# Kernel optimization log

Measured on AMD Instinct MI355X. Metric: run time of the kernel, lower is better.

Reference implementation:

```python
import jax, jax.numpy as jnp
import numpy as np

B, T, E, H = 4, 1024, 768, 12
HD = E // H                      # 64
R = 2                            # lora rank
LORA_SCALE = 1.0 / R             # loralib default lora_alpha=1 -> alpha/r
NUM_BUCKETS, MAX_DIST = 320, 800


def _rel_bucket(rel):
    nb = NUM_BUCKETS // 2                      # 160
    buckets = (rel > 0).astype(jnp.int32) * nb
    rel = jnp.abs(rel)
    max_exact = nb // 2                        # 80
    is_small = rel < max_exact
    log_ratio = jnp.log(jnp.maximum(rel, 1).astype(jnp.float32) / max_exact)
    large = max_exact + (log_ratio / np.log(MAX_DIST / max_exact) * (nb - max_exact)).astype(jnp.int32)
    large = jnp.minimum(large, nb - 1)
    return buckets + jnp.where(is_small, rel, large)


def setup_inputs() -> dict:
    key = jax.random.key(0)
    ks = jax.random.split(key, 22)
    s = 0.02
    w = lambda k, shape: jax.random.normal(k, shape, jnp.float32) * s
    return {
        "hidden_states": jax.random.normal(ks[0], (B, T, E), jnp.float32),
        "Wq": w(ks[1], (E, E)), "bq": w(ks[2], (E,)),
        "Wk": w(ks[3], (E, E)), "bk": w(ks[4], (E,)),
        "Wv": w(ks[5], (E, E)), "bv": w(ks[6], (E,)),
        "Aq": w(ks[7], (R, E)), "Bq": w(ks[8], (E, R)),
        "Ak": w(ks[9], (R, E)), "Bk": w(ks[10], (E, R)),
        "Av": w(ks[11], (R, E)), "Bv": w(ks[12], (E, R)),
        "Wo": w(ks[13], (E, E)), "bo": w(ks[14], (E,)),
        "Wg": w(ks[15], (8, HD)), "bg": w(ks[16], (8,)),
        "gru_const": jnp.ones((1, H, 1, 1), jnp.float32),
        "rel_embed": w(ks[17], (NUM_BUCKETS, H)),
    }


def reference(hidden_states, Wq, bq, Wk, bk, Wv, bv,
              Aq, Bq, Ak, Bk, Av, Bv, Wo, bo, Wg, bg, gru_const, rel_embed):
    Bsz, Tq, _ = hidden_states.shape
    # --- relative position bias [H, T, T] ---
    pos = jnp.arange(Tq)
    bucket = _rel_bucket(pos[None, :] - pos[:, None])
    pos_bias = rel_embed[bucket].transpose(2, 0, 1)
    # --- dynamic gate from hidden states, per head/position ---
    g = hidden_states.reshape(Bsz, Tq, H, HD).transpose(0, 2, 1, 3)      # [B,H,T,hd]
    gp = jnp.einsum('bhtd,ed->bhte', g, Wg) + bg                          # [B,H,T,8]
    gp = gp.reshape(Bsz, H, Tq, 2, 4).sum(-1)                             # [B,H,T,2]
    gates = jax.nn.sigmoid(gp)
    gate_a, gate_b = gates[..., :1], gates[..., 1:]
    gate = gate_a * (gate_b * gru_const - 1.0) + 2.0                      # [B,H,T,1]
    gated_bias = gate * pos_bias[None]                                    # [B,H,T,T]
    # --- projections: original double-applies q/k/v_proj (proj+LoRA, then
    #     again inside F.multi_head_attention_forward via separate proj weights) ---
    lin = lambda x, W, b: jnp.einsum('bte,oe->bto', x, W) + b
    lora = lambda x, A, Bm: jnp.einsum('bte,re,or->bto', x, A, Bm) * LORA_SCALE
    x = hidden_states
    q1 = lin(x, Wq, bq) + lora(x, Aq, Bq)
    k1 = lin(x, Wk, bk) + lora(x, Ak, Bk)
    v1 = lin(x, Wv, bv) + lora(x, Av, Bv)
    q = lin(q1, Wq, bq) * (HD ** -0.5)
    k = lin(k1, Wk, bk)
    v = lin(v1, Wv, bv)
    qh = q.reshape(Bsz, Tq, H, HD).transpose(0, 2, 1, 3)
    kh = k.reshape(Bsz, Tq, H, HD).transpose(0, 2, 1, 3)
    vh = v.reshape(Bsz, Tq, H, HD).transpose(0, 2, 1, 3)
    scores = jnp.einsum('bhqd,bhkd->bhqk', qh, kh) + gated_bias
    attn = jax.nn.softmax(scores, axis=-1)
    ctx = jnp.einsum('bhqk,bhkd->bhqd', attn, vh)
    out = ctx.transpose(0, 2, 1, 3).reshape(Bsz, Tq, E)
    return jnp.einsum('bte,oe->bto', out, Wo) + bo
```

## Files before the change

### kernel.cpp

```cpp
#include <hip/hip_runtime.h>
#include <math.h>

#define TT 1024
#define EE 768
#define HH 12

typedef __attribute__((ext_vector_type(8))) __bf16 bf16x8;
typedef __attribute__((ext_vector_type(4))) float f32x4;

__device__ __forceinline__ unsigned short f2b(float f) {
    unsigned int u = __float_as_uint(f);
    unsigned int r = (u + 0x7fffu + ((u >> 16) & 1u)) >> 16;
    return (unsigned short)r;
}

#define GLD16(gsrc, ldst) \
    __builtin_amdgcn_global_load_lds( \
        (const __attribute__((address_space(1))) unsigned int*)(gsrc), \
        (__attribute__((address_space(3))) unsigned int*)(ldst), 16, 0, 0)

__global__ __launch_bounds__(256)
void prep_k(const float* __restrict__ hs, const float* __restrict__ Wq,
            const float* __restrict__ Wk, const float* __restrict__ Wv,
            const float* __restrict__ Wo, unsigned short* __restrict__ out) {
    size_t i = 4 * (size_t)(blockIdx.x * 256 + threadIdx.x);
    if (i >= 5505024) return;
    const float* src;
    if (i < 3145728)      src = hs + i;
    else if (i < 3735552) src = Wq + (i - 3145728);
    else if (i < 4325376) src = Wk + (i - 3735552);
    else if (i < 4915200) src = Wv + (i - 4325376);
    else                  src = Wo + (i - 4915200);
    float4 f = *(const float4*)src;
    unsigned int lo = (unsigned int)f2b(f.x) | ((unsigned int)f2b(f.y) << 16);
    unsigned int hi = (unsigned int)f2b(f.z) | ((unsigned int)f2b(f.w) << 16);
    uint2 p; p.x = lo; p.y = hi;
    *(uint2*)&out[i] = p;
}

__global__ void biastab_k(const float* __restrict__ rel_embed,
                          float* __restrict__ biasTab) {
    int idx = blockIdx.x * 256 + threadIdx.x;
    if (idx >= 2047 * 12) return;
    int h = idx % 12;
    int rr = idx / 12;
    int rel = rr - 1023;
    int base = rel > 0 ? 160 : 0;
    int ar = rel < 0 ? -rel : rel;
    int bkt;
    if (ar < 80) {
        bkt = base + ar;
    } else {
        double lr = log((double)ar / 80.0);
        int large = 80 + (int)(lr / log(10.0) * 80.0);
        if (large > 159) large = 159;
        bkt = base + large;
    }
    biasTab[h * 2048 + rr] = rel_embed[bkt * 12 + h];
}

__global__ __launch_bounds__(256)
void gates_k(const float* __restrict__ hs, const float* __restrict__ Wg,
             const float* __restrict__ bg, const float* __restrict__ gru,
             float* __restrict__ gate) {
    __shared__ float WgS[8][64];
    __shared__ float bgS[8];
    __shared__ float gcS[12];
    const int tid = threadIdx.x;
    for (int i = tid; i < 512; i += 256) WgS[i >> 6][i & 63] = Wg[i];
    if (tid < 8)  bgS[tid] = bg[tid];
    if (tid < 12) gcS[tid] = gru[tid];
    __syncthreads();
    int idx = blockIdx.x * 256 + tid;
    int t = idx & 1023;
    int h = (idx >> 10) % 12;
    int b = idx / (12 * 1024);
    const float* gp = hs + ((size_t)(b * TT + t)) * EE + h * 64;
    float acc[8];
    #pragma unroll
    for (int e = 0; e < 8; ++e) acc[e] = 0.f;
    #pragma unroll
    for (int d4 = 0; d4 < 64; d4 += 4) {
        float4 u = *(const float4*)(gp + d4);
        float gv[4] = {u.x, u.y, u.z, u.w};
        #pragma unroll
        for (int j = 0; j < 4; ++j) {
            #pragma unroll
            for (int e = 0; e < 8; ++e) acc[e] += gv[j] * WgS[e][d4 + j];
        }
    }
    float s0 = acc[0] + acc[1] + acc[2] + acc[3] + bgS[0] + bgS[1] + bgS[2] + bgS[3];
    float s1 = acc[4] + acc[5] + acc[6] + acc[7] + bgS[4] + bgS[5] + bgS[6] + bgS[7];
    float ga = 1.f / (1.f + __expf(-s0));
    float gb = 1.f / (1.f + __expf(-s1));
    gate[idx] = ga * (gb * gcS[h] - 1.0f) + 2.0f;
}

__global__ __launch_bounds__(64)
void lora_down_k(const float* __restrict__ x,
                 const float* __restrict__ Aq, const float* __restrict__ Ak,
                 const float* __restrict__ Av, float* __restrict__ xA) {
    const int m = blockIdx.x;
    const int lane = threadIdx.x;
    const float* xp = x + (size_t)m * EE;
    float s[6] = {0.f, 0.f, 0.f, 0.f, 0.f, 0.f};
    for (int c = lane * 4; c < EE; c += 256) {
        float4 u = *(const float4*)(xp + c);
        float xv[4] = {u.x, u.y, u.z, u.w};
        #pragma unroll
        for (int j = 0; j < 4; ++j) {
            int e = c + j;
            s[0] += xv[j] * Aq[e];       s[1] += xv[j] * Aq[EE + e];
            s[2] += xv[j] * Ak[e];       s[3] += xv[j] * Ak[EE + e];
            s[4] += xv[j] * Av[e];       s[5] += xv[j] * Av[EE + e];
        }
    }
    #pragma unroll
    for (int off = 32; off > 0; off >>= 1) {
        #pragma unroll
        for (int i = 0; i < 6; ++i) s[i] += __shfl_down(s[i], off, 64);
    }
    if (lane == 0) {
        const int M2 = 4096 * 2;
        xA[m * 2 + 0] = s[0];            xA[m * 2 + 1] = s[1];
        xA[M2 + m * 2 + 0] = s[2];       xA[M2 + m * 2 + 1] = s[3];
        xA[2 * M2 + m * 2 + 0] = s[4];   xA[2 * M2 + m * 2 + 1] = s[5];
    }
}

template<int MODE>
__global__ __launch_bounds__(256, 2)
void gemm_k(const unsigned short* __restrict__ Aall,
            const unsigned short* __restrict__ W0b, const unsigned short* __restrict__ W1b,
            const unsigned short* __restrict__ W2b,
            const float* __restrict__ b0, const float* __restrict__ b1, const float* __restrict__ b2,
            const float* __restrict__ xA,
            const float* __restrict__ Bm0, const float* __restrict__ Bm1, const float* __restrict__ Bm2,
            void* __restrict__ out) {
    __shared__ unsigned short At[128 * 32];
    __shared__ unsigned short Bt[128 * 32];
    const int tid = threadIdx.x;
    const int bx = blockIdx.x, by = blockIdx.y;

    int sel, row0, col0;
    if (MODE == 0)      { sel = bx / 6;  col0 = (bx % 6) * 128; row0 = by * 128; }
    else if (MODE == 1) { sel = by / 32; col0 = bx * 128;       row0 = by * 128; }
    else                { sel = 0;       col0 = bx * 128;       row0 = by * 128; }
    const unsigned short* Wb = sel == 0 ? W0b : (sel == 1 ? W1b : W2b);
    const float* bias = sel == 0 ? b0 : (sel == 1 ? b1 : b2);
    float scale = (MODE == 1 && sel == 0) ? 0.125f : 1.0f;

    const int lane = tid & 63, wv = tid >> 6;
    const int wm = (wv & 1) * 64, wn = (wv >> 1) * 64;
    const int l15 = lane & 15, g8 = (lane >> 4) * 8;
    const int lr = lane >> 2, lc = (lane & 3) * 8;

    f32x4 zero4 = {0.f, 0.f, 0.f, 0.f};
    f32x4 acc[4][4];
    #pragma unroll
    for (int i = 0; i < 4; ++i)
        #pragma unroll
        for (int j = 0; j < 4; ++j) acc[i][j] = zero4;

    const int c0 = wv * 2, c1 = wv * 2 + 1;
    const unsigned short* Abase0 = Aall + (size_t)(row0 + c0 * 16 + lr) * EE + lc;
    const unsigned short* Abase1 = Aall + (size_t)(row0 + c1 * 16 + lr) * EE + lc;
    const unsigned short* Bbase0 = Wb + (size_t)(col0 + c0 * 16 + lr) * EE + lc;
    const unsigned short* Bbase1 = Wb + (size_t)(col0 + c1 * 16 + lr) * EE + lc;

    for (int kt = 0; kt < 768; kt += 32) {
        GLD16(Abase0 + kt, &At[c0 * 512]);
        GLD16(Abase1 + kt, &At[c1 * 512]);
        GLD16(Bbase0 + kt, &Bt[c0 * 512]);
        GLD16(Bbase1 + kt, &Bt[c1 * 512]);
        __syncthreads();
        bf16x8 af[4], bf[4];
        #pragma unroll
        for (int mt = 0; mt < 4; ++mt) af[mt] = *(const bf16x8*)&At[(wm + mt * 16 + l15) * 32 + g8];
        #pragma unroll
        for (int nt = 0; nt < 4; ++nt) bf[nt] = *(const bf16x8*)&Bt[(wn + nt * 16 + l15) * 32 + g8];
        #pragma unroll
        for (int mt = 0; mt < 4; ++mt)
            #pragma unroll
            for (int nt = 0; nt < 4; ++nt)
                acc[mt][nt] = __builtin_amdgcn_mfma_f32_16x16x32_bf16(af[mt], bf[nt], acc[mt][nt], 0, 0, 0);
        __syncthreads();
    }

    const float* Lbase = (MODE == 0) ? (xA + sel * 8192) : nullptr;
    const float* BmSel = (MODE == 0) ? (sel == 0 ? Bm0 : (sel == 1 ? Bm1 : Bm2)) : nullptr;
    const int g4 = (lane >> 4) * 4;
    #pragma unroll
    for (int mt = 0; mt < 4; ++mt) {
        #pragma unroll
        for (int r = 0; r < 4; ++r) {
            size_t grow = (size_t)row0 + wm + mt * 16 + g4 + r;
            float l0 = 0.f, l1 = 0.f;
            if (MODE == 0) { l0 = Lbase[grow * 2]; l1 = Lbase[grow * 2 + 1]; }
            #pragma unroll
            for (int nt = 0; nt < 4; ++nt) {
                int ncol = col0 + wn + nt * 16 + l15;
                float c = (acc[mt][nt][r] + bias[ncol]) * scale;
                if (MODE == 0) c += 0.5f * (l0 * BmSel[ncol * 2] + l1 * BmSel[ncol * 2 + 1]);
                if (MODE == 0) {
                    ((unsigned short*)out)[(size_t)sel * 4096 * EE + grow * EE + ncol] = f2b(c);
                } else if (MODE == 1) {
                    ((unsigned short*)out)[grow * EE + ncol] = f2b(c);
                } else {
                    ((float*)out)[grow * EE + ncol] = c;
                }
            }
        }
    }
}

__global__ __launch_bounds__(256)
void vT_k(const unsigned short* __restrict__ vb, unsigned short* __restrict__ Vtg) {
    __shared__ unsigned short Vs[64 * 72];
    const int tid = threadIdx.x;
    const int tt = blockIdx.x, h = blockIdx.y, b = blockIdx.z;
    const int r = tid >> 3, cc = (tid & 7) * 8;
    #pragma unroll
    for (int i = 0; i < 2; ++i) {
        int row = i * 32 + r;
        const unsigned short* vp = vb + (size_t)(b * TT + tt * 64 + row) * EE + h * 64 + cc;
        *(uint4*)&Vs[row * 72 + cc] = *(const uint4*)vp;
    }
    __syncthreads();
    #pragma unroll
    for (int i = 0; i < 2; ++i) {
        int d = i * 32 + r;
        unsigned short tmp[8] __attribute__((aligned(16)));
        #pragma unroll
        for (int j = 0; j < 8; ++j) tmp[j] = Vs[(cc + j) * 72 + d];
        *(uint4*)&Vtg[((size_t)(b * HH + h) * 64 + d) * TT + tt * 64 + cc] = *(const uint4*)tmp;
    }
}

__global__ __launch_bounds__(256, 3)
void attn_k(const unsigned short* __restrict__ qb, const unsigned short* __restrict__ kb,
            const unsigned short* __restrict__ Vtg, const float* __restrict__ gate,
            const float* __restrict__ biasTab, unsigned short* __restrict__ ctx) {
    __shared__ unsigned short Qs[64 * 72];
    __shared__ unsigned short Ks[64 * 72];
    __shared__ unsigned short Vt[64 * 72];
    __shared__ unsigned short Ps[64 * 72];
    __shared__ float btabS[2048];
    const int tid = threadIdx.x;
    const int qt = blockIdx.x, h = blockIdx.y, b = blockIdx.z;

    for (int i = tid; i < 2047; i += 256) btabS[i] = biasTab[h * 2048 + i];

    const int srow = tid >> 2, scol = (tid & 3) * 16;
    {
        const unsigned short* qp = qb + ((size_t)(b * TT + qt * 64 + srow)) * EE + h * 64 + scol;
        *(uint4*)&Qs[srow * 72 + scol]     = *(const uint4*)qp;
        *(uint4*)&Qs[srow * 72 + scol + 8] = *(const uint4*)(qp + 8);
    }
    const int lane = tid & 63, wv = tid >> 6;
    const int m0 = wv * 16;
    const int l15 = lane & 15, g = lane >> 4;

    float li[4];
    f32x4 zero4 = {0.f, 0.f, 0.f, 0.f};
    f32x4 oa[4];
    #pragma unroll
    for (int r = 0; r < 4; ++r) li[r] = 0.f;
    #pragma unroll
    for (int nt = 0; nt < 4; ++nt) oa[nt] = zero4;
    float gv[4];
    #pragma unroll
    for (int r = 0; r < 4; ++r)
        gv[r] = gate[((size_t)(b * HH + h)) * TT + qt * 64 + m0 + 4 * g + r];
    const unsigned short* vrow = Vtg + ((size_t)(b * HH + h) * 64 + srow) * TT;
    __syncthreads();

    for (int kt = 0; kt < 16; ++kt) {
        {
            const unsigned short* kp = kb + ((size_t)(b * TT + kt * 64 + srow)) * EE + h * 64 + scol;
            *(uint4*)&Ks[srow * 72 + scol]     = *(const uint4*)kp;
            *(uint4*)&Ks[srow * 72 + scol + 8] = *(const uint4*)(kp + 8);
            const unsigned short* vp = vrow + kt * 64 + scol;
            *(uint4*)&Vt[srow * 72 + scol]     = *(const uint4*)vp;
            *(uint4*)&Vt[srow * 72 + scol + 8] = *(const uint4*)(vp + 8);
        }
        __syncthreads();
        f32x4 sa[4];
        #pragma unroll
        for (int nt = 0; nt < 4; ++nt) sa[nt] = zero4;
        bf16x8 aq0 = *(const bf16x8*)&Qs[(m0 + l15) * 72 + g * 8];
        bf16x8 aq1 = *(const bf16x8*)&Qs[(m0 + l15) * 72 + 32 + g * 8];
        #pragma unroll
        for (int nt = 0; nt < 4; ++nt) {
            bf16x8 bk0 = *(const bf16x8*)&Ks[(nt * 16 + l15) * 72 + g * 8];
            bf16x8 bk1 = *(const bf16x8*)&Ks[(nt * 16 + l15) * 72 + 32 + g * 8];
            sa[nt] = __builtin_amdgcn_mfma_f32_16x16x32_bf16(aq0, bk0, sa[nt], 0, 0, 0);
            sa[nt] = __builtin_amdgcn_mfma_f32_16x16x32_bf16(aq1, bk1, sa[nt], 0, 0, 0);
        }
        #pragma unroll
        for (int nt = 0; nt < 4; ++nt) {
            int ibase = kt * 64 + nt * 16 + l15 + 1023 - qt * 64 - m0 - 4 * g;
            #pragma unroll
            for (int r = 0; r < 4; ++r) {
                float e = __expf(sa[nt][r] + gv[r] * btabS[ibase - r]);
                li[r] += e;
                Ps[(m0 + 4 * g + r) * 72 + nt * 16 + l15] = f2b(e);
            }
        }
        bf16x8 ap0 = *(const bf16x8*)&Ps[(m0 + l15) * 72 + g * 8];
        bf16x8 ap1 = *(const bf16x8*)&Ps[(m0 + l15) * 72 + 32 + g * 8];
        #pragma unroll
        for (int nt = 0; nt < 4; ++nt) {
            bf16x8 bv0 = *(const bf16x8*)&Vt[(nt * 16 + l15) * 72 + g * 8];
            bf16x8 bv1 = *(const bf16x8*)&Vt[(nt * 16 + l15) * 72 + 32 + g * 8];
            oa[nt] = __builtin_amdgcn_mfma_f32_16x16x32_bf16(ap0, bv0, oa[nt], 0, 0, 0);
            oa[nt] = __builtin_amdgcn_mfma_f32_16x16x32_bf16(ap1, bv1, oa[nt], 0, 0, 0);
        }
        __syncthreads();
    }
    #pragma unroll
    for (int r = 0; r < 4; ++r) {
        #pragma unroll
        for (int msk = 1; msk < 16; msk <<= 1)
            li[r] += __shfl_xor(li[r], msk, 16);
    }
    #pragma unroll
    for (int nt = 0; nt < 4; ++nt)
        #pragma unroll
        for (int r = 0; r < 4; ++r)
            Ks[(m0 + 4 * g + r) * 72 + nt * 16 + l15] = f2b(oa[nt][r] / li[r]);
    __syncthreads();
    {
        unsigned short* cp = ctx + ((size_t)(b * TT + qt * 64 + srow)) * EE + h * 64 + scol;
        *(uint4*)cp       = *(const uint4*)&Ks[srow * 72 + scol];
        *(uint4*)(cp + 8) = *(const uint4*)&Ks[srow * 72 + scol + 8];
    }
}

extern "C" void kernel_launch(void* const* d_in, const int* in_sizes, int n_in,
                              void* d_out, int out_size, void* d_ws, size_t ws_size,
                              hipStream_t stream) {
    const float* hs  = (const float*)d_in[0];
    const float* Wq  = (const float*)d_in[1];
    const float* bq  = (const float*)d_in[2];
    const float* Wk  = (const float*)d_in[3];
    const float* bk  = (const float*)d_in[4];
    const float* Wv  = (const float*)d_in[5];
    const float* bv  = (const float*)d_in[6];
    const float* Aq  = (const float*)d_in[7];
    const float* Bq  = (const float*)d_in[8];
    const float* Ak  = (const float*)d_in[9];
    const float* Bk  = (const float*)d_in[10];
    const float* Av  = (const float*)d_in[11];
    const float* Bv  = (const float*)d_in[12];
    const float* Wo  = (const float*)d_in[13];
    const float* bo  = (const float*)d_in[14];
    const float* Wg  = (const float*)d_in[15];
    const float* bg  = (const float*)d_in[16];
    const float* gru = (const float*)d_in[17];
    const float* rel = (const float*)d_in[18];

    float* ws = (float*)d_ws;
    float* gate    = ws;
    float* biasTab = gate + 49152;
    float* xA      = biasTab + 24576;
    unsigned short* hsb   = (unsigned short*)(xA + 24576);
    unsigned short* Wqb   = hsb + 3145728;
    unsigned short* Wkb   = Wqb + 589824;
    unsigned short* Wvb   = Wkb + 589824;
    unsigned short* Wob   = Wvb + 589824;
    unsigned short* qkv1b = Wob + 589824;
    unsigned short* qkvb  = qkv1b + 3 * 3145728;
    unsigned short* ctxb  = qkv1b;
    unsigned short* Vtg   = qkv1b + 3145728;

    prep_k<<<5376, 256, 0, stream>>>(hs, Wq, Wk, Wv, Wo, hsb);
    biastab_k<<<96, 256, 0, stream>>>(rel, biasTab);
    gates_k<<<192, 256, 0, stream>>>(hs, Wg, bg, gru, gate);
    lora_down_k<<<4096, 64, 0, stream>>>(hs, Aq, Ak, Av, xA);

    gemm_k<0><<<dim3(18, 32), 256, 0, stream>>>(hsb, Wqb, Wkb, Wvb, bq, bk, bv,
                                                xA, Bq, Bk, Bv, qkv1b);
    gemm_k<1><<<dim3(6, 96), 256, 0, stream>>>(qkv1b, Wqb, Wkb, Wvb, bq, bk, bv,
                                               nullptr, nullptr, nullptr, nullptr, qkvb);

    vT_k<<<dim3(16, 12, 4), 256, 0, stream>>>(qkvb + 2 * 3145728, Vtg);

    attn_k<<<dim3(16, 12, 4), 256, 0, stream>>>(qkvb, qkvb + 3145728, Vtg,
                                                gate, biasTab, ctxb);

    gemm_k<2><<<dim3(6, 32), 256, 0, stream>>>(ctxb, Wob, Wob, Wob, bo, bo, bo,
                                               nullptr, nullptr, nullptr, nullptr, d_out);
}
```

Measured before the change: 241.4 us.

## Fold double projection into precomputed W·W weights and fuse setup kernels

The two chained q/k/v projections are folded algebraically: W2 = W·W is computed by a small weight GEMM, together with a combined bias W·b+b and LoRA factor W·B, so only one large activation GEMM is needed. The four prep kernels (bf16 convert, bias table, gates, LoRA down) are merged into one multi-role setup kernel. The V transpose is fused into the projection epilogue through strided stores. This removes a full 4096x2304x768 GEMM and several launches, at the cost of a weight-side GEMM per call and extra bf16 rounding of the product weights.

```diff
diff --git a/kernel.cpp b/kernel.cpp
--- a/kernel.cpp
+++ b/kernel.cpp
@@ -20,154 +20,264 @@
         (__attribute__((address_space(3))) unsigned int*)(ldst), 16, 0, 0)
 
 __global__ __launch_bounds__(256)
-void prep_k(const float* __restrict__ hs, const float* __restrict__ Wq,
-            const float* __restrict__ Wk, const float* __restrict__ Wv,
-            const float* __restrict__ Wo, unsigned short* __restrict__ out) {
-    size_t i = 4 * (size_t)(blockIdx.x * 256 + threadIdx.x);
-    if (i >= 5505024) return;
-    const float* src;
-    if (i < 3145728)      src = hs + i;
-    else if (i < 3735552) src = Wq + (i - 3145728);
-    else if (i < 4325376) src = Wk + (i - 3735552);
-    else if (i < 4915200) src = Wv + (i - 4325376);
-    else                  src = Wo + (i - 4915200);
-    float4 f = *(const float4*)src;
-    unsigned int lo = (unsigned int)f2b(f.x) | ((unsigned int)f2b(f.y) << 16);
-    unsigned int hi = (unsigned int)f2b(f.z) | ((unsigned int)f2b(f.w) << 16);
-    uint2 p; p.x = lo; p.y = hi;
-    *(uint2*)&out[i] = p;
-}
-
-__global__ void biastab_k(const float* __restrict__ rel_embed,
-                          float* __restrict__ biasTab) {
-    int idx = blockIdx.x * 256 + threadIdx.x;
-    if (idx >= 2047 * 12) return;
-    int h = idx % 12;
-    int rr = idx / 12;
-    int rel = rr - 1023;
-    int base = rel > 0 ? 160 : 0;
-    int ar = rel < 0 ? -rel : rel;
-    int bkt;
-    if (ar < 80) {
-        bkt = base + ar;
+void setup_k(const float* __restrict__ hs,
+             const float* __restrict__ Wq, const float* __restrict__ Wk,
+             const float* __restrict__ Wv, const float* __restrict__ Wo,
+             const float* __restrict__ bq, const float* __restrict__ bk,
+             const float* __restrict__ bv,
+             const float* __restrict__ Aq, const float* __restrict__ Ak,
+             const float* __restrict__ Av,
+             const float* __restrict__ Bq, const float* __restrict__ Bk,
+             const float* __restrict__ Bv,
+             const float* __restrict__ Wg, const float* __restrict__ bg,
+             const float* __restrict__ gru, const float* __restrict__ rel,
+             unsigned short* __restrict__ hsb, unsigned short* __restrict__ Wall_b,
+             unsigned short* __restrict__ WT_all,
+             float* __restrict__ xA, float* __restrict__ gate,
+             float* __restrict__ biasTab, float* __restrict__ bias2,
+             float* __restrict__ B2) {
+    __shared__ __align__(16) char smem[34816];
+    const int bid = blockIdx.x, tid = threadIdx.x;
+
+    if (bid < 4096) {
+        float* rowF = (float*)smem;
+        float* WgS  = rowF + 768;
+        float* bgS  = WgS + 512;
+        float* gpS  = bgS + 8;
+        float* redS = gpS + 96;
+        const int m = bid;
+        const float* xrow = hs + (size_t)m * EE;
+        if (tid < 192) {
+            float4 f = ((const float4*)xrow)[tid];
+            rowF[tid * 4 + 0] = f.x; rowF[tid * 4 + 1] = f.y;
+            rowF[tid * 4 + 2] = f.z; rowF[tid * 4 + 3] = f.w;
+            unsigned int lo = (unsigned int)f2b(f.x) | ((unsigned int)f2b(f.y) << 16);
+            unsigned int hi = (unsigned int)f2b(f.z) | ((unsigned int)f2b(f.w) << 16);
+            uint2 p; p.x = lo; p.y = hi;
+            *(uint2*)&hsb[(size_t)m * EE + tid * 4] = p;
+        }
+        for (int i = tid; i < 512; i += 256) WgS[i] = Wg[i];
+        if (tid < 8) bgS[tid] = bg[tid];
+        __syncthreads();
+        float s[6] = {0.f, 0.f, 0.f, 0.f, 0.f, 0.f};
+        #pragma unroll
+        for (int j = 0; j < 3; ++j) {
+            int e = tid * 3 + j;
+            float xv = rowF[e];
+            s[0] += xv * Aq[e]; s[1] += xv * Aq[EE + e];
+            s[2] += xv * Ak[e]; s[3] += xv * Ak[EE + e];
+            s[4] += xv * Av[e]; s[5] += xv * Av[EE + e];
+        }
+        #pragma unroll
+        for (int off = 32; off > 0; off >>= 1)
+            #pragma unroll
+            for (int i = 0; i < 6; ++i) s[i] += __shfl_down(s[i], off, 64);
+        if ((tid & 63) == 0)
+            #pragma unroll
+            for (int i = 0; i < 6; ++i) redS[(tid >> 6) * 6 + i] = s[i];
+        if (tid < 96) {
+            int h = tid >> 3, e = tid & 7;
+            float acc = 0.f;
+            #pragma unroll 16
+            for (int d = 0; d < 64; ++d) acc += rowF[h * 64 + d] * WgS[e * 64 + d];
+            gpS[h * 8 + e] = acc + bgS[e];
+        }
+        __syncthreads();
+        if (tid < 6) {
+            float v = redS[tid] + redS[6 + tid] + redS[12 + tid] + redS[18 + tid];
+            int sel = tid >> 1, r = tid & 1;
+            xA[sel * 8192 + m * 2 + r] = v;
+        }
+        if (tid < 12) {
+            int h = tid;
+            float s0 = gpS[h * 8 + 0] + gpS[h * 8 + 1] + gpS[h * 8 + 2] + gpS[h * 8 + 3];
+            float s1 = gpS[h * 8 + 4] + gpS[h * 8 + 5] + gpS[h * 8 + 6] + gpS[h * 8 + 7];
+            float ga = 1.f / (1.f + __expf(-s0));
+            float gb = 1.f / (1.f + __expf(-s1));
+            int b = m >> 10, tp = m & 1023;
+            gate[((size_t)b * HH + h) * TT + tp] = ga * (gb * gru[h] - 1.0f) + 2.0f;
+        }
+    } else if (bid < 5248) {
+        size_t base = (size_t)(bid - 4096) * 2048 + tid * 8;
+        int mat = (int)(base / 589824);
+        size_t local = base % 589824;
+        const float* S = mat == 0 ? Wq : (mat == 1 ? Wk : (mat == 2 ? Wv : Wo));
+        float4 a = *(const float4*)&S[local];
+        float4 c = *(const float4*)&S[local + 4];
+        unsigned short hb[8] __attribute__((aligned(16)));
+        hb[0] = f2b(a.x); hb[1] = f2b(a.y); hb[2] = f2b(a.z); hb[3] = f2b(a.w);
+        hb[4] = f2b(c.x); hb[5] = f2b(c.y); hb[6] = f2b(c.z); hb[7] = f2b(c.w);
+        *(uint4*)&Wall_b[base] = *(const uint4*)hb;
+    } else if (bid < 5356) {
+        unsigned short* Ts = (unsigned short*)smem;
+        int v = bid - 5248;
+        int mat = v / 36, tile = v % 36;
+        int tr = tile / 6, tc = tile % 6;
+        const float* S = mat == 0 ? Wq : (mat == 1 ? Wk : Wv);
+        #pragma unroll
+        for (int i = 0; i < 16; ++i) {
+            int idx = i * 256 + tid;
+            int row = idx >> 5, col4 = (idx & 31) * 4;
+            float4 f = *(const float4*)&S[(size_t)(tr * 128 + row) * EE + tc * 128 + col4];
+            Ts[(col4 + 0) * 136 + row] = f2b(f.x);
+            Ts[(col4 + 1) * 136 + row] = f2b(f.y);
+            Ts[(col4 + 2) * 136 + row] = f2b(f.z);
+            Ts[(col4 + 3) * 136 + row] = f2b(f.w);
+        }
+        __syncthreads();
+        unsigned short* dst = WT_all + (size_t)mat * 589824;
+        #pragma unroll
+        for (int i = 0; i < 8; ++i) {
+            int idx = i * 256 + tid;
+            int rr = idx >> 4, cg = (idx & 15) * 8;
+            *(uint4*)&dst[(size_t)(tc * 128 + rr) * EE + tr * 128 + cg] =
+                *(const uint4*)&Ts[rr * 136 + cg];
+        }
+    } else if (bid < 5452) {
+        int idx = (bid - 5356) * 256 + tid;
+        if (idx < 2047 * 12) {
+            int h = idx % 12;
+            int rr = idx / 12;
+            int relv = rr - 1023;
+            int base = relv > 0 ? 160 : 0;
+            int ar = relv < 0 ? -relv : relv;
+            int bkt;
+            if (ar < 80) bkt = base + ar;
+            else {
+                double lr = log((double)ar / 80.0);
+                int large = 80 + (int)(lr / log(10.0) * 80.0);
+                if (large > 159) large = 159;
+                bkt = base + large;
+            }
+            biasTab[h * 2048 + rr] = rel[bkt * 12 + h];
+        }
     } else {
-        double lr = log((double)ar / 80.0);
-        int large = 80 + (int)(lr / log(10.0) * 80.0);
-        if (large > 159) large = 159;
-        bkt = base + large;
-    }
-    biasTab[h * 2048 + rr] = rel_embed[bkt * 12 + h];
-}
-
-__global__ __launch_bounds__(256)
-void gates_k(const float* __restrict__ hs, const float* __restrict__ Wg,
-             const float* __restrict__ bg, const float* __restrict__ gru,
-             float* __restrict__ gate) {
-    __shared__ float WgS[8][64];
-    __shared__ float bgS[8];
-    __shared__ float gcS[12];
+        float* bvS = (float*)smem;
+        float* BmS = bvS + 768;
+        int v = bid - 5452;
+        int sel = v / 4, nb = (v % 4) * 192;
+        const float* W = sel == 0 ? Wq : (sel == 1 ? Wk : Wv);
+        const float* bvec = sel == 0 ? bq : (sel == 1 ? bk : bv);
+        const float* Bm = sel == 0 ? Bq : (sel == 1 ? Bk : Bv);
+        for (int i = tid; i < 768; i += 256) bvS[i] = bvec[i];
+        for (int i = tid; i < 1536; i += 256) BmS[i] = Bm[i];
+        __syncthreads();
+        if (tid < 192) {
+            int n = nb + tid;
+            const float* Wrow = W + (size_t)n * EE;
+            float a0 = 0.f, a1 = 0.f, a2 = 0.f;
+            for (int o = 0; o < EE; o += 4) {
+                float4 w = *(const float4*)&Wrow[o];
+                a0 += w.x * bvS[o] + w.y * bvS[o + 1] + w.z * bvS[o + 2] + w.w * bvS[o + 3];
+                a1 += w.x * BmS[o * 2] + w.y * BmS[o * 2 + 2] + w.z * BmS[o * 2 + 4] + w.w * BmS[o * 2 + 6];
+                a2 += w.x * BmS[o * 2 + 1] + w.y * BmS[o * 2 + 3] + w.z * BmS[o * 2 + 5] + w.w * BmS[o * 2 + 7];
+            }
+            bias2[sel * 768 + n] = a0 + bvS[n];
+            B2[sel * 1536 + n * 2 + 0] = a1;
+            B2[sel * 1536 + n * 2 + 1] = a2;
+        }
+    }
+}
+
+__global__ __launch_bounds__(256, 2)
+void wgemm_k(const unsigned short* __restrict__ Wall_b,
+             const unsigned short* __restrict__ WT_all,
+             unsigned short* __restrict__ W2_all) {
+    __shared__ unsigned short At[128 * 32];
+    __shared__ unsigned short Bt[128 * 32];
     const int tid = threadIdx.x;
-    for (int i = tid; i < 512; i += 256) WgS[i >> 6][i & 63] = Wg[i];
-    if (tid < 8)  bgS[tid] = bg[tid];
-    if (tid < 12) gcS[tid] = gru[tid];
-    __syncthreads();
-    int idx = blockIdx.x * 256 + tid;
-    int t = idx & 1023;
-    int h = (idx >> 10) % 12;
-    int b = idx / (12 * 1024);
-    const float* gp = hs + ((size_t)(b * TT + t)) * EE + h * 64;
-    float acc[8];
-    #pragma unroll
-    for (int e = 0; e < 8; ++e) acc[e] = 0.f;
-    #pragma unroll
-    for (int d4 = 0; d4 < 64; d4 += 4) {
-        float4 u = *(const float4*)(gp + d4);
-        float gv[4] = {u.x, u.y, u.z, u.w};
-        #pragma unroll
-        for (int j = 0; j < 4; ++j) {
-            #pragma unroll
-            for (int e = 0; e < 8; ++e) acc[e] += gv[j] * WgS[e][d4 + j];
-        }
-    }
-    float s0 = acc[0] + acc[1] + acc[2] + acc[3] + bgS[0] + bgS[1] + bgS[2] + bgS[3];
-    float s1 = acc[4] + acc[5] + acc[6] + acc[7] + bgS[4] + bgS[5] + bgS[6] + bgS[7];
-    float ga = 1.f / (1.f + __expf(-s0));
-    float gb = 1.f / (1.f + __expf(-s1));
-    gate[idx] = ga * (gb * gcS[h] - 1.0f) + 2.0f;
-}
-
-__global__ __launch_bounds__(64)
-void lora_down_k(const float* __restrict__ x,
-                 const float* __restrict__ Aq, const float* __restrict__ Ak,
-                 const float* __restrict__ Av, float* __restrict__ xA) {
-    const int m = blockIdx.x;
-    const int lane = threadIdx.x;
-    const float* xp = x + (size_t)m * EE;
-    float s[6] = {0.f, 0.f, 0.f, 0.f, 0.f, 0.f};
-    for (int c = lane * 4; c < EE; c += 256) {
-        float4 u = *(const float4*)(xp + c);
-        float xv[4] = {u.x, u.y, u.z, u.w};
-        #pragma unroll
-        for (int j = 0; j < 4; ++j) {
-            int e = c + j;
-            s[0] += xv[j] * Aq[e];       s[1] += xv[j] * Aq[EE + e];
-            s[2] += xv[j] * Ak[e];       s[3] += xv[j] * Ak[EE + e];
-            s[4] += xv[j] * Av[e];       s[5] += xv[j] * Av[EE + e];
-        }
-    }
-    #pragma unroll
-    for (int off = 32; off > 0; off >>= 1) {
-        #pragma unroll
-        for (int i = 0; i < 6; ++i) s[i] += __shfl_down(s[i], off, 64);
-    }
-    if (lane == 0) {
-        const int M2 = 4096 * 2;
-        xA[m * 2 + 0] = s[0];            xA[m * 2 + 1] = s[1];
-        xA[M2 + m * 2 + 0] = s[2];       xA[M2 + m * 2 + 1] = s[3];
-        xA[2 * M2 + m * 2 + 0] = s[4];   xA[2 * M2 + m * 2 + 1] = s[5];
-    }
+    const int bxx = blockIdx.x;
+    const int sel = bxx / 36, tile = bxx % 36;
+    const int row0 = (tile / 6) * 128, col0 = (tile % 6) * 128;
+    const unsigned short* A = Wall_b + (size_t)sel * 589824;
+    const unsigned short* Bw = WT_all + (size_t)sel * 589824;
+
+    const int lane = tid & 63, wv = tid >> 6;
+    const int wm = (wv & 1) * 64, wn = (wv >> 1) * 64;
+    const int l15 = lane & 15, g8 = (lane >> 4) * 8;
+    const int lr = lane >> 2, lc = (lane & 3) * 8;
+    const int c0 = wv * 2, c1 = wv * 2 + 1;
+    const unsigned short* Abase0 = A + (size_t)(row0 + c0 * 16 + lr) * EE + lc;
+    const unsigned short* Abase1 = A + (size_t)(row0 + c1 * 16 + lr) * EE + lc;
+    const unsigned short* Bbase0 = Bw + (size_t)(col0 + c0 * 16 + lr) * EE + lc;
+    const unsigned short* Bbase1 = Bw + (size_t)(col0 + c1 * 16 + lr) * EE + lc;
+
+    f32x4 zero4 = {0.f, 0.f, 0.f, 0.f};
+    f32x4 acc[4][4];
+    #pragma unroll
+    for (int i = 0; i < 4; ++i)
+        #pragma unroll
+        for (int j = 0; j < 4; ++j) acc[i][j] = zero4;
+
+    for (int kt = 0; kt < 768; kt += 32) {
+        GLD16(Abase0 + kt, &At[c0 * 512]);
+        GLD16(Abase1 + kt, &At[c1 * 512]);
+        GLD16(Bbase0 + kt, &Bt[c0 * 512]);
+        GLD16(Bbase1 + kt, &Bt[c1 * 512]);
+        __syncthreads();
+        bf16x8 af[4], bf[4];
+        #pragma unroll
+        for (int mt = 0; mt < 4; ++mt) af[mt] = *(const bf16x8*)&At[(wm + mt * 16 + l15) * 32 + g8];
+        #pragma unroll
+        for (int nt = 0; nt < 4; ++nt) bf[nt] = *(const bf16x8*)&Bt[(wn + nt * 16 + l15) * 32 + g8];
+        #pragma unroll
+        for (int mt = 0; mt < 4; ++mt)
+            #pragma unroll
+            for (int nt = 0; nt < 4; ++nt)
+                acc[mt][nt] = __builtin_amdgcn_mfma_f32_16x16x32_bf16(af[mt], bf[nt], acc[mt][nt], 0, 0, 0);
+        __syncthreads();
+    }
+    unsigned short* out = W2_all + (size_t)sel * 589824;
+    const int g4 = (lane >> 4) * 4;
+    #pragma unroll
+    for (int mt = 0; mt < 4; ++mt)
+        #pragma unroll
+        for (int r = 0; r < 4; ++r) {
+            int grow = row0 + wm + mt * 16 + g4 + r;
+            #pragma unroll
+            for (int nt = 0; nt < 4; ++nt) {
+                int ncol = col0 + wn + nt * 16 + l15;
+                out[(size_t)grow * EE + ncol] = f2b(acc[mt][nt][r]);
+            }
+        }
 }
 
 template<int MODE>
 __global__ __launch_bounds__(256, 2)
 void gemm_k(const unsigned short* __restrict__ Aall,
-            const unsigned short* __restrict__ W0b, const unsigned short* __restrict__ W1b,
-            const unsigned short* __restrict__ W2b,
-            const float* __restrict__ b0, const float* __restrict__ b1, const float* __restrict__ b2,
-            const float* __restrict__ xA,
-            const float* __restrict__ Bm0, const float* __restrict__ Bm1, const float* __restrict__ Bm2,
-            void* __restrict__ out) {
+            const unsigned short* __restrict__ Wb_base,
+            const float* __restrict__ bias_base,
+            const float* __restrict__ xA, const float* __restrict__ B2,
+            unsigned short* __restrict__ qb, unsigned short* __restrict__ kb,
+            unsigned short* __restrict__ Vtg, float* __restrict__ outf) {
     __shared__ unsigned short At[128 * 32];
     __shared__ unsigned short Bt[128 * 32];
     const int tid = threadIdx.x;
     const int bx = blockIdx.x, by = blockIdx.y;
-
     int sel, row0, col0;
-    if (MODE == 0)      { sel = bx / 6;  col0 = (bx % 6) * 128; row0 = by * 128; }
-    else if (MODE == 1) { sel = by / 32; col0 = bx * 128;       row0 = by * 128; }
-    else                { sel = 0;       col0 = bx * 128;       row0 = by * 128; }
-    const unsigned short* Wb = sel == 0 ? W0b : (sel == 1 ? W1b : W2b);
-    const float* bias = sel == 0 ? b0 : (sel == 1 ? b1 : b2);
-    float scale = (MODE == 1 && sel == 0) ? 0.125f : 1.0f;
+    if (MODE == 0) { sel = bx / 6; col0 = (bx % 6) * 128; row0 = by * 128; }
+    else           { sel = 0;      col0 = bx * 128;       row0 = by * 128; }
+    const unsigned short* Wb = Wb_base + (size_t)sel * 589824;
+    const float* bias = bias_base + sel * 768;
+    const float scale = (MODE == 0 && sel == 0) ? 0.125f : 1.0f;
 
     const int lane = tid & 63, wv = tid >> 6;
     const int wm = (wv & 1) * 64, wn = (wv >> 1) * 64;
     const int l15 = lane & 15, g8 = (lane >> 4) * 8;
     const int lr = lane >> 2, lc = (lane & 3) * 8;
-
-    f32x4 zero4 = {0.f, 0.f, 0.f, 0.f};
-    f32x4 acc[4][4];
-    #pragma unroll
-    for (int i = 0; i < 4; ++i)
-        #pragma unroll
-        for (int j = 0; j < 4; ++j) acc[i][j] = zero4;
-
     const int c0 = wv * 2, c1 = wv * 2 + 1;
     const unsigned short* Abase0 = Aall + (size_t)(row0 + c0 * 16 + lr) * EE + lc;
     const unsigned short* Abase1 = Aall + (size_t)(row0 + c1 * 16 + lr) * EE + lc;
     const unsigned short* Bbase0 = Wb + (size_t)(col0 + c0 * 16 + lr) * EE + lc;
     const unsigned short* Bbase1 = Wb + (size_t)(col0 + c1 * 16 + lr) * EE + lc;
 
+    f32x4 zero4 = {0.f, 0.f, 0.f, 0.f};
+    f32x4 acc[4][4];
+    #pragma unroll
+    for (int i = 0; i < 4; ++i)
+        #pragma unroll
+        for (int j = 0; j < 4; ++j) acc[i][j] = zero4;
+
     for (int kt = 0; kt < 768; kt += 32) {
         GLD16(Abase0 + kt, &At[c0 * 512]);
         GLD16(Abase1 + kt, &At[c1 * 512]);
@@ -188,7 +298,7 @@
     }
 
     const float* Lbase = (MODE == 0) ? (xA + sel * 8192) : nullptr;
-    const float* BmSel = (MODE == 0) ? (sel == 0 ? Bm0 : (sel == 1 ? Bm1 : Bm2)) : nullptr;
+    const float* B2s   = (MODE == 0) ? (B2 + sel * 1536) : nullptr;
     const int g4 = (lane >> 4) * 4;
     #pragma unroll
     for (int mt = 0; mt < 4; ++mt) {
@@ -200,40 +310,21 @@
             #pragma unroll
             for (int nt = 0; nt < 4; ++nt) {
                 int ncol = col0 + wn + nt * 16 + l15;
-                float c = (acc[mt][nt][r] + bias[ncol]) * scale;
-                if (MODE == 0) c += 0.5f * (l0 * BmSel[ncol * 2] + l1 * BmSel[ncol * 2 + 1]);
+                float c = acc[mt][nt][r] + bias[ncol];
                 if (MODE == 0) {
-                    ((unsigned short*)out)[(size_t)sel * 4096 * EE + grow * EE + ncol] = f2b(c);
-                } else if (MODE == 1) {
-                    ((unsigned short*)out)[grow * EE + ncol] = f2b(c);
+                    c = (c + 0.5f * (l0 * B2s[ncol * 2] + l1 * B2s[ncol * 2 + 1])) * scale;
+                    if (sel == 0)      qb[grow * EE + ncol] = f2b(c);
+                    else if (sel == 1) kb[grow * EE + ncol] = f2b(c);
+                    else {
+                        int b = (int)(grow >> 10), t = (int)(grow & 1023);
+                        int h = ncol >> 6, d = ncol & 63;
+                        Vtg[(((size_t)b * HH + h) * 64 + d) * TT + t] = f2b(c);
+                    }
                 } else {
-                    ((float*)out)[grow * EE + ncol] = c;
+                    outf[grow * EE + ncol] = c;
                 }
             }
         }
-    }
-}
-
-__global__ __launch_bounds__(256)
-void vT_k(const unsigned short* __restrict__ vb, unsigned short* __restrict__ Vtg) {
-    __shared__ unsigned short Vs[64 * 72];
-    const int tid = threadIdx.x;
-    const int tt = blockIdx.x, h = blockIdx.y, b = blockIdx.z;
-    const int r = tid >> 3, cc = (tid & 7) * 8;
-    #pragma unroll
-    for (int i = 0; i < 2; ++i) {
-        int row = i * 32 + r;
-        const unsigned short* vp = vb + (size_t)(b * TT + tt * 64 + row) * EE + h * 64 + cc;
-        *(uint4*)&Vs[row * 72 + cc] = *(const uint4*)vp;
-    }
-    __syncthreads();
-    #pragma unroll
-    for (int i = 0; i < 2; ++i) {
-        int d = i * 32 + r;
-        unsigned short tmp[8] __attribute__((aligned(16)));
-        #pragma unroll
-        for (int j = 0; j < 8; ++j) tmp[j] = Vs[(cc + j) * 72 + d];
-        *(uint4*)&Vtg[((size_t)(b * HH + h) * 64 + d) * TT + tt * 64 + cc] = *(const uint4*)tmp;
     }
 }
 
@@ -364,31 +455,25 @@
     float* gate    = ws;
     float* biasTab = gate + 49152;
     float* xA      = biasTab + 24576;
-    unsigned short* hsb   = (unsigned short*)(xA + 24576);
-    unsigned short* Wqb   = hsb + 3145728;
-    unsigned short* Wkb   = Wqb + 589824;
-    unsigned short* Wvb   = Wkb + 589824;
-    unsigned short* Wob   = Wvb + 589824;
-    unsigned short* qkv1b = Wob + 589824;
-    unsigned short* qkvb  = qkv1b + 3 * 3145728;
-    unsigned short* ctxb  = qkv1b;
-    unsigned short* Vtg   = qkv1b + 3145728;
-
-    prep_k<<<5376, 256, 0, stream>>>(hs, Wq, Wk, Wv, Wo, hsb);
-    biastab_k<<<96, 256, 0, stream>>>(rel, biasTab);
-    gates_k<<<192, 256, 0, stream>>>(hs, Wg, bg, gru, gate);
-    lora_down_k<<<4096, 64, 0, stream>>>(hs, Aq, Ak, Av, xA);
-
-    gemm_k<0><<<dim3(18, 32), 256, 0, stream>>>(hsb, Wqb, Wkb, Wvb, bq, bk, bv,
-                                                xA, Bq, Bk, Bv, qkv1b);
-    gemm_k<1><<<dim3(6, 96), 256, 0, stream>>>(qkv1b, Wqb, Wkb, Wvb, bq, bk, bv,
-                                               nullptr, nullptr, nullptr, nullptr, qkvb);
-
-    vT_k<<<dim3(16, 12, 4), 256, 0, stream>>>(qkvb + 2 * 3145728, Vtg);
-
-    attn_k<<<dim3(16, 12, 4), 256, 0, stream>>>(qkvb, qkvb + 3145728, Vtg,
-                                                gate, biasTab, ctxb);
-
-    gemm_k<2><<<dim3(6, 32), 256, 0, stream>>>(ctxb, Wob, Wob, Wob, bo, bo, bo,
-                                               nullptr, nullptr, nullptr, nullptr, d_out);
-}
+    float* bias2   = xA + 24576;
+    float* B2      = bias2 + 2304;
+    unsigned short* hsb    = (unsigned short*)(B2 + 4608);
+    unsigned short* Wall_b = hsb + 3145728;
+    unsigned short* WT_all = Wall_b + 4 * 589824;
+    unsigned short* W2_all = WT_all + 3 * 589824;
+    unsigned short* qb     = W2_all + 3 * 589824;
+    unsigned short* kb     = qb + 3145728;
+    unsigned short* Vtg    = kb + 3145728;
+    unsigned short* ctxb   = Vtg + 3145728;
+
+    setup_k<<<5464, 256, 0, stream>>>(hs, Wq, Wk, Wv, Wo, bq, bk, bv,
+                                      Aq, Ak, Av, Bq, Bk, Bv, Wg, bg, gru, rel,
+                                      hsb, Wall_b, WT_all, xA, gate, biasTab, bias2, B2);
+    wgemm_k<<<108, 256, 0, stream>>>(Wall_b, WT_all, W2_all);
+    gemm_k<0><<<dim3(18, 32), 256, 0, stream>>>(hsb, W2_all, bias2, xA, B2,
+                                                qb, kb, Vtg, nullptr);
+    attn_k<<<dim3(16, 12, 4), 256, 0, stream>>>(qb, kb, Vtg, gate, biasTab, ctxb);
+    gemm_k<2><<<dim3(6, 32), 256, 0, stream>>>(ctxb, Wall_b + 3 * 589824, bo,
+                                               nullptr, nullptr, nullptr, nullptr, nullptr,
+                                               (float*)d_out);
+}
```

After: 256.3 us. 6.2% more time.

## Fold double q/k/v projection into precomputed W·W weight products

Applied to the files above, without the earlier changes.

Because each projection is applied twice with the same weights, the change precomputes W2 = W·W (and the folded bias W·b + b and LoRA up-projection W·B) with a small weight-only GEMM, then runs a single activation GEMM per projection instead of two. This removes one full 4096x768x2304 GEMM and the intermediate qkv1 round-trip through memory. The cost is a transpose kernel, an extra 768^3 weight GEMM per call, and rounding W2 to bf16, which changes the numerics slightly.

```diff
diff --git a/kernel.cpp b/kernel.cpp
--- a/kernel.cpp
+++ b/kernel.cpp
@@ -38,6 +38,36 @@
     *(uint2*)&out[i] = p;
 }
 
+__global__ __launch_bounds__(256)
+void wT_k(const float* __restrict__ Wq, const float* __restrict__ Wk,
+          const float* __restrict__ Wv, unsigned short* __restrict__ WT_all) {
+    __shared__ unsigned short Ts[128 * 136];
+    const int v = blockIdx.x;
+    const int mat = v / 36, tile = v % 36;
+    const int tr = tile / 6, tc = tile % 6;
+    const float* S = mat == 0 ? Wq : (mat == 1 ? Wk : Wv);
+    const int tid = threadIdx.x;
+    #pragma unroll
+    for (int i = 0; i < 16; ++i) {
+        int idx = i * 256 + tid;
+        int row = idx >> 5, col4 = (idx & 31) * 4;
+        float4 f = *(const float4*)&S[(size_t)(tr * 128 + row) * EE + tc * 128 + col4];
+        Ts[(col4 + 0) * 136 + row] = f2b(f.x);
+        Ts[(col4 + 1) * 136 + row] = f2b(f.y);
+        Ts[(col4 + 2) * 136 + row] = f2b(f.z);
+        Ts[(col4 + 3) * 136 + row] = f2b(f.w);
+    }
+    __syncthreads();
+    unsigned short* dst = WT_all + (size_t)mat * 589824;
+    #pragma unroll
+    for (int i = 0; i < 8; ++i) {
+        int idx = i * 256 + tid;
+        int rr = idx >> 4, cg = (idx & 15) * 8;
+        *(uint4*)&dst[(size_t)(tc * 128 + rr) * EE + tr * 128 + cg] =
+            *(const uint4*)&Ts[rr * 136 + cg];
+    }
+}
+
 __global__ void biastab_k(const float* __restrict__ rel_embed,
                           float* __restrict__ biasTab) {
     int idx = blockIdx.x * 256 + threadIdx.x;
@@ -121,39 +151,69 @@
         for (int i = 0; i < 6; ++i) s[i] += __shfl_down(s[i], off, 64);
     }
     if (lane == 0) {
-        const int M2 = 4096 * 2;
-        xA[m * 2 + 0] = s[0];            xA[m * 2 + 1] = s[1];
-        xA[M2 + m * 2 + 0] = s[2];       xA[M2 + m * 2 + 1] = s[3];
-        xA[2 * M2 + m * 2 + 0] = s[4];   xA[2 * M2 + m * 2 + 1] = s[5];
-    }
-}
-
-template<int MODE>
+        xA[m * 2 + 0] = s[0];                xA[m * 2 + 1] = s[1];
+        xA[8192 + m * 2 + 0] = s[2];         xA[8192 + m * 2 + 1] = s[3];
+        xA[16384 + m * 2 + 0] = s[4];        xA[16384 + m * 2 + 1] = s[5];
+    }
+}
+
+__global__ __launch_bounds__(256)
+void bias2_k(const float* __restrict__ Wq, const float* __restrict__ Wk,
+             const float* __restrict__ Wv,
+             const float* __restrict__ bq, const float* __restrict__ bk,
+             const float* __restrict__ bv,
+             const float* __restrict__ Bq, const float* __restrict__ Bk,
+             const float* __restrict__ Bv,
+             float* __restrict__ bias2, float* __restrict__ B2) {
+    __shared__ float bvS[768];
+    __shared__ float BmS[1536];
+    const int tid = threadIdx.x;
+    int v = blockIdx.x;
+    int sel = v / 4, nb = (v % 4) * 192;
+    const float* W = sel == 0 ? Wq : (sel == 1 ? Wk : Wv);
+    const float* bvec = sel == 0 ? bq : (sel == 1 ? bk : bv);
+    const float* Bm = sel == 0 ? Bq : (sel == 1 ? Bk : Bv);
+    for (int i = tid; i < 768; i += 256) bvS[i] = bvec[i];
+    for (int i = tid; i < 1536; i += 256) BmS[i] = Bm[i];
+    __syncthreads();
+    if (tid < 192) {
+        int n = nb + tid;
+        const float* Wrow = W + (size_t)n * EE;
+        float a0 = 0.f, a1 = 0.f, a2 = 0.f;
+        for (int o = 0; o < EE; o += 4) {
+            float4 w = *(const float4*)&Wrow[o];
+            a0 += w.x * bvS[o] + w.y * bvS[o + 1] + w.z * bvS[o + 2] + w.w * bvS[o + 3];
+            a1 += w.x * BmS[o * 2] + w.y * BmS[o * 2 + 2] + w.z * BmS[o * 2 + 4] + w.w * BmS[o * 2 + 6];
+            a2 += w.x * BmS[o * 2 + 1] + w.y * BmS[o * 2 + 3] + w.z * BmS[o * 2 + 5] + w.w * BmS[o * 2 + 7];
+        }
+        bias2[sel * 768 + n] = a0 + bvS[n];
+        B2[sel * 1536 + n * 2 + 0] = a1;
+        B2[sel * 1536 + n * 2 + 1] = a2;
+    }
+}
+
 __global__ __launch_bounds__(256, 2)
-void gemm_k(const unsigned short* __restrict__ Aall,
-            const unsigned short* __restrict__ W0b, const unsigned short* __restrict__ W1b,
-            const unsigned short* __restrict__ W2b,
-            const float* __restrict__ b0, const float* __restrict__ b1, const float* __restrict__ b2,
-            const float* __restrict__ xA,
-            const float* __restrict__ Bm0, const float* __restrict__ Bm1, const float* __restrict__ Bm2,
-            void* __restrict__ out) {
+void wgemm_k(const unsigned short* __restrict__ Wall_b,
+             const unsigned short* __restrict__ WT_all,
+             unsigned short* __restrict__ W2_all) {
     __shared__ unsigned short At[128 * 32];
     __shared__ unsigned short Bt[128 * 32];
     const int tid = threadIdx.x;
-    const int bx = blockIdx.x, by = blockIdx.y;
-
-    int sel, row0, col0;
-    if (MODE == 0)      { sel = bx / 6;  col0 = (bx % 6) * 128; row0 = by * 128; }
-    else if (MODE == 1) { sel = by / 32; col0 = bx * 128;       row0 = by * 128; }
-    else                { sel = 0;       col0 = bx * 128;       row0 = by * 128; }
-    const unsigned short* Wb = sel == 0 ? W0b : (sel == 1 ? W1b : W2b);
-    const float* bias = sel == 0 ? b0 : (sel == 1 ? b1 : b2);
-    float scale = (MODE == 1 && sel == 0) ? 0.125f : 1.0f;
+    const int bxx = blockIdx.x;
+    const int sel = bxx / 36, tile = bxx % 36;
+    const int row0 = (tile / 6) * 128, col0 = (tile % 6) * 128;
+    const unsigned short* A = Wall_b + (size_t)sel * 589824;
+    const unsigned short* Bw = WT_all + (size_t)sel * 589824;
 
     const int lane = tid & 63, wv = tid >> 6;
     const int wm = (wv & 1) * 64, wn = (wv >> 1) * 64;
     const int l15 = lane & 15, g8 = (lane >> 4) * 8;
     const int lr = lane >> 2, lc = (lane & 3) * 8;
+    const int c0 = wv * 2, c1 = wv * 2 + 1;
+    const unsigned short* Abase0 = A + (size_t)(row0 + c0 * 16 + lr) * EE + lc;
+    const unsigned short* Abase1 = A + (size_t)(row0 + c1 * 16 + lr) * EE + lc;
+    const unsigned short* Bbase0 = Bw + (size_t)(col0 + c0 * 16 + lr) * EE + lc;
+    const unsigned short* Bbase1 = Bw + (size_t)(col0 + c1 * 16 + lr) * EE + lc;
 
     f32x4 zero4 = {0.f, 0.f, 0.f, 0.f};
     f32x4 acc[4][4];
@@ -162,12 +222,73 @@
         #pragma unroll
         for (int j = 0; j < 4; ++j) acc[i][j] = zero4;
 
+    for (int kt = 0; kt < 768; kt += 32) {
+        GLD16(Abase0 + kt, &At[c0 * 512]);
+        GLD16(Abase1 + kt, &At[c1 * 512]);
+        GLD16(Bbase0 + kt, &Bt[c0 * 512]);
+        GLD16(Bbase1 + kt, &Bt[c1 * 512]);
+        __syncthreads();
+        bf16x8 af[4], bf[4];
+        #pragma unroll
+        for (int mt = 0; mt < 4; ++mt) af[mt] = *(const bf16x8*)&At[(wm + mt * 16 + l15) * 32 + g8];
+        #pragma unroll
+        for (int nt = 0; nt < 4; ++nt) bf[nt] = *(const bf16x8*)&Bt[(wn + nt * 16 + l15) * 32 + g8];
+        #pragma unroll
+        for (int mt = 0; mt < 4; ++mt)
+            #pragma unroll
+            for (int nt = 0; nt < 4; ++nt)
+                acc[mt][nt] = __builtin_amdgcn_mfma_f32_16x16x32_bf16(af[mt], bf[nt], acc[mt][nt], 0, 0, 0);
+        __syncthreads();
+    }
+    unsigned short* out = W2_all + (size_t)sel * 589824;
+    const int g4 = (lane >> 4) * 4;
+    #pragma unroll
+    for (int mt = 0; mt < 4; ++mt)
+        #pragma unroll
+        for (int r = 0; r < 4; ++r) {
+            int grow = row0 + wm + mt * 16 + g4 + r;
+            #pragma unroll
+            for (int nt = 0; nt < 4; ++nt) {
+                int ncol = col0 + wn + nt * 16 + l15;
+                out[(size_t)grow * EE + ncol] = f2b(acc[mt][nt][r]);
+            }
+        }
+}
+
+__global__ __launch_bounds__(256, 2)
+void qkv_gemm_k(const unsigned short* __restrict__ Aall,
+                const unsigned short* __restrict__ W2_all,
+                const float* __restrict__ bias2,
+                const float* __restrict__ xA, const float* __restrict__ B2,
+                unsigned short* __restrict__ qb, unsigned short* __restrict__ kb,
+                unsigned short* __restrict__ vb) {
+    __shared__ unsigned short At[128 * 32];
+    __shared__ unsigned short Bt[128 * 32];
+    const int tid = threadIdx.x;
+    const int bx = blockIdx.x, by = blockIdx.y;
+    const int sel = bx / 6;
+    const int col0 = (bx % 6) * 128, row0 = by * 128;
+    const unsigned short* Wb = W2_all + (size_t)sel * 589824;
+    const float* bias = bias2 + sel * 768;
+    const float scale = (sel == 0) ? 0.125f : 1.0f;
+
+    const int lane = tid & 63, wv = tid >> 6;
+    const int wm = (wv & 1) * 64, wn = (wv >> 1) * 64;
+    const int l15 = lane & 15, g8 = (lane >> 4) * 8;
+    const int lr = lane >> 2, lc = (lane & 3) * 8;
     const int c0 = wv * 2, c1 = wv * 2 + 1;
     const unsigned short* Abase0 = Aall + (size_t)(row0 + c0 * 16 + lr) * EE + lc;
     const unsigned short* Abase1 = Aall + (size_t)(row0 + c1 * 16 + lr) * EE + lc;
     const unsigned short* Bbase0 = Wb + (size_t)(col0 + c0 * 16 + lr) * EE + lc;
     const unsigned short* Bbase1 = Wb + (size_t)(col0 + c1 * 16 + lr) * EE + lc;
 
+    f32x4 zero4 = {0.f, 0.f, 0.f, 0.f};
+    f32x4 acc[4][4];
+    #pragma unroll
+    for (int i = 0; i < 4; ++i)
+        #pragma unroll
+        for (int j = 0; j < 4; ++j) acc[i][j] = zero4;
+
     for (int kt = 0; kt < 768; kt += 32) {
         GLD16(Abase0 + kt, &At[c0 * 512]);
         GLD16(Abase1 + kt, &At[c1 * 512]);
@@ -187,28 +308,22 @@
         __syncthreads();
     }
 
-    const float* Lbase = (MODE == 0) ? (xA + sel * 8192) : nullptr;
-    const float* BmSel = (MODE == 0) ? (sel == 0 ? Bm0 : (sel == 1 ? Bm1 : Bm2)) : nullptr;
+    unsigned short* dst = sel == 0 ? qb : (sel == 1 ? kb : vb);
+    const float* Lbase = xA + sel * 8192;
+    const float* B2s   = B2 + sel * 1536;
     const int g4 = (lane >> 4) * 4;
     #pragma unroll
     for (int mt = 0; mt < 4; ++mt) {
         #pragma unroll
         for (int r = 0; r < 4; ++r) {
             size_t grow = (size_t)row0 + wm + mt * 16 + g4 + r;
-            float l0 = 0.f, l1 = 0.f;
-            if (MODE == 0) { l0 = Lbase[grow * 2]; l1 = Lbase[grow * 2 + 1]; }
+            float l0 = Lbase[grow * 2], l1 = Lbase[grow * 2 + 1];
             #pragma unroll
             for (int nt = 0; nt < 4; ++nt) {
                 int ncol = col0 + wn + nt * 16 + l15;
-                float c = (acc[mt][nt][r] + bias[ncol]) * scale;
-                if (MODE == 0) c += 0.5f * (l0 * BmSel[ncol * 2] + l1 * BmSel[ncol * 2 + 1]);
-                if (MODE == 0) {
-                    ((unsigned short*)out)[(size_t)sel * 4096 * EE + grow * EE + ncol] = f2b(c);
-                } else if (MODE == 1) {
-                    ((unsigned short*)out)[grow * EE + ncol] = f2b(c);
-                } else {
-                    ((float*)out)[grow * EE + ncol] = c;
-                }
+                float c = (acc[mt][nt][r] + bias[ncol]
+                           + 0.5f * (l0 * B2s[ncol * 2] + l1 * B2s[ncol * 2 + 1])) * scale;
+                dst[grow * EE + ncol] = f2b(c);
             }
         }
     }
@@ -335,6 +450,64 @@
         *(uint4*)cp       = *(const uint4*)&Ks[srow * 72 + scol];
         *(uint4*)(cp + 8) = *(const uint4*)&Ks[srow * 72 + scol + 8];
     }
+}
+
+__global__ __launch_bounds__(256, 2)
+void out_gemm_k(const unsigned short* __restrict__ Aall,
+                const unsigned short* __restrict__ Wob,
+                const float* __restrict__ bo, float* __restrict__ outf) {
+    __shared__ unsigned short At[128 * 32];
+    __shared__ unsigned short Bt[128 * 32];
+    const int tid = threadIdx.x;
+    const int col0 = blockIdx.x * 128, row0 = blockIdx.y * 128;
+
+    const int lane = tid & 63, wv = tid >> 6;
+    const int wm = (wv & 1) * 64, wn = (wv >> 1) * 64;
+    const int l15 = lane & 15, g8 = (lane >> 4) * 8;
+    const int lr = lane >> 2, lc = (lane & 3) * 8;
+    const int c0 = wv * 2, c1 = wv * 2 + 1;
+    const unsigned short* Abase0 = Aall + (size_t)(row0 + c0 * 16 + lr) * EE + lc;
+    const unsigned short* Abase1 = Aall + (size_t)(row0 + c1 * 16 + lr) * EE + lc;
+    const unsigned short* Bbase0 = Wob + (size_t)(col0 + c0 * 16 + lr) * EE + lc;
+    const unsigned short* Bbase1 = Wob + (size_t)(col0 + c1 * 16 + lr) * EE + lc;
+
+    f32x4 zero4 = {0.f, 0.f, 0.f, 0.f};
+    f32x4 acc[4][4];
+    #pragma unroll
+    for (int i = 0; i < 4; ++i)
+        #pragma unroll
+        for (int j = 0; j < 4; ++j) acc[i][j] = zero4;
+
+    for (int kt = 0; kt < 768; kt += 32) {
+        GLD16(Abase0 + kt, &At[c0 * 512]);
+        GLD16(Abase1 + kt, &At[c1 * 512]);
+        GLD16(Bbase0 + kt, &Bt[c0 * 512]);
+        GLD16(Bbase1 + kt, &Bt[c1 * 512]);
+        __syncthreads();
+        bf16x8 af[4], bf[4];
+        #pragma unroll
+        for (int mt = 0; mt < 4; ++mt) af[mt] = *(const bf16x8*)&At[(wm + mt * 16 + l15) * 32 + g8];
+        #pragma unroll
+        for (int nt = 0; nt < 4; ++nt) bf[nt] = *(const bf16x8*)&Bt[(wn + nt * 16 + l15) * 32 + g8];
+        #pragma unroll
+        for (int mt = 0; mt < 4; ++mt)
+            #pragma unroll
+            for (int nt = 0; nt < 4; ++nt)
+                acc[mt][nt] = __builtin_amdgcn_mfma_f32_16x16x32_bf16(af[mt], bf[nt], acc[mt][nt], 0, 0, 0);
+        __syncthreads();
+    }
+    const int g4 = (lane >> 4) * 4;
+    #pragma unroll
+    for (int mt = 0; mt < 4; ++mt)
+        #pragma unroll
+        for (int r = 0; r < 4; ++r) {
+            size_t grow = (size_t)row0 + wm + mt * 16 + g4 + r;
+            #pragma unroll
+            for (int nt = 0; nt < 4; ++nt) {
+                int ncol = col0 + wn + nt * 16 + l15;
+                outf[grow * EE + ncol] = acc[mt][nt][r] + bo[ncol];
+            }
+        }
 }
 
 extern "C" void kernel_launch(void* const* d_in, const int* in_sizes, int n_in,
@@ -364,31 +537,28 @@
     float* gate    = ws;
     float* biasTab = gate + 49152;
     float* xA      = biasTab + 24576;
-    unsigned short* hsb   = (unsigned short*)(xA + 24576);
-    unsigned short* Wqb   = hsb + 3145728;
-    unsigned short* Wkb   = Wqb + 589824;
-    unsigned short* Wvb   = Wkb + 589824;
-    unsigned short* Wob   = Wvb + 589824;
-    unsigned short* qkv1b = Wob + 589824;
-    unsigned short* qkvb  = qkv1b + 3 * 3145728;
-    unsigned short* ctxb  = qkv1b;
-    unsigned short* Vtg   = qkv1b + 3145728;
+    float* bias2   = xA + 24576;
+    float* B2      = bias2 + 2304;
+    unsigned short* hsb    = (unsigned short*)(B2 + 4608);
+    unsigned short* Wall_b = hsb + 3145728;
+    unsigned short* WT_all = Wall_b + 4 * 589824;
+    unsigned short* W2_all = WT_all + 3 * 589824;
+    unsigned short* qb     = W2_all + 3 * 589824;
+    unsigned short* kb     = qb + 3145728;
+    unsigned short* vb     = kb + 3145728;
+    unsigned short* Vtg    = vb + 3145728;
+    unsigned short* ctxb   = Vtg + 3145728;
 
     prep_k<<<5376, 256, 0, stream>>>(hs, Wq, Wk, Wv, Wo, hsb);
-    biastab_k<<<96, 256, 0, stream>>>(rel, biasTab);
+    wT_k<<<108, 256, 0, stream>>>(Wq, Wk, Wv, WT_all);
     gates_k<<<192, 256, 0, stream>>>(hs, Wg, bg, gru, gate);
     lora_down_k<<<4096, 64, 0, stream>>>(hs, Aq, Ak, Av, xA);
-
-    gemm_k<0><<<dim3(18, 32), 256, 0, stream>>>(hsb, Wqb, Wkb, Wvb, bq, bk, bv,
-                                                xA, Bq, Bk, Bv, qkv1b);
-    gemm_k<1><<<dim3(6, 96), 256, 0, stream>>>(qkv1b, Wqb, Wkb, Wvb, bq, bk, bv,
-                                               nullptr, nullptr, nullptr, nullptr, qkvb);
-
-    vT_k<<<dim3(16, 12, 4), 256, 0, stream>>>(qkvb + 2 * 3145728, Vtg);
-
-    attn_k<<<dim3(16, 12, 4), 256, 0, stream>>>(qkvb, qkvb + 3145728, Vtg,
-                                                gate, biasTab, ctxb);
-
-    gemm_k<2><<<dim3(6, 32), 256, 0, stream>>>(ctxb, Wob, Wob, Wob, bo, bo, bo,
-                                               nullptr, nullptr, nullptr, nullptr, d_out);
-}
+    biastab_k<<<96, 256, 0, stream>>>(rel, biasTab);
+    bias2_k<<<12, 256, 0, stream>>>(Wq, Wk, Wv, bq, bk, bv, Bq, Bk, Bv, bias2, B2);
+
+    wgemm_k<<<108, 256, 0, stream>>>(Wall_b, WT_all, W2_all);
+    qkv_gemm_k<<<dim3(18, 32), 256, 0, stream>>>(hsb, W2_all, bias2, xA, B2, qb, kb, vb);
+    vT_k<<<dim3(16, 12, 4), 256, 0, stream>>>(vb, Vtg);
+    attn_k<<<dim3(16, 12, 4), 256, 0, stream>>>(qb, kb, Vtg, gate, biasTab, ctxb);
+    out_gemm_k<<<dim3(6, 32), 256, 0, stream>>>(ctxb, Wall_b + 3 * 589824, bo, (float*)d_out);
+}
```

New measurement: 260.6 us. +7.9%, slower.
